# Kernel tuning notes

Hardware: AMD Instinct MI355X
Metric: run time of the kernel (lower is better)

Reference implementation:

```python
import jax, jax.numpy as jnp
import numpy as np

B, N1, N2 = 4, 2048, 8192
F_IN, F_OUT = 256, 256
K = 3          # PyG knn_interpolate default
BN_EPS = 1e-5


def linear_bn(x, W, b, gamma, beta):
    # Linear + BatchNorm1d (training mode: batch stats over B*N per feature)
    h = jnp.einsum('bni,io->bno', x, W) + b
    mean = h.mean(axis=(0, 1))
    var = h.var(axis=(0, 1))
    xhat = (h - mean) * jax.lax.rsqrt(var + BN_EPS)
    return gamma * xhat + beta


def knn_interpolate(f1, p1, p2):
    # f1: [N1,F], p1: [N1,3], p2: [N2,3] -> [N2,F]
    d2 = jnp.sum((p2[:, None, :] - p1[None, :, :]) ** 2, axis=-1)  # [N2,N1]
    neg_d2, idx = jax.lax.top_k(-d2, K)                            # k smallest
    w = 1.0 / jnp.maximum(-neg_d2, 1e-16)                          # [N2,K]
    fk = f1[idx]                                                   # [N2,K,F]
    return jnp.sum(w[..., None] * fk, axis=1) / jnp.sum(w, axis=1, keepdims=True)


def setup_inputs() -> dict:
    key = jax.random.key(0)
    ks = jax.random.split(key, 10)
    return {
        'features_1': jax.random.normal(ks[0], (B, N1, F_IN), jnp.float32),
        'positions_1': jax.random.uniform(ks[1], (B, N1, 3), jnp.float32),
        'batch_1': jnp.repeat(jnp.arange(B, dtype=jnp.int64), N1),
        'features_2': jax.random.normal(ks[2], (B, N2, F_IN), jnp.float32),
        'positions_2': jax.random.uniform(ks[3], (B, N2, 3), jnp.float32),
        'batch_2': jnp.repeat(jnp.arange(B, dtype=jnp.int64), N2),
        'W1': jax.random.normal(ks[4], (F_IN, F_OUT), jnp.float32) * (1.0 / np.sqrt(F_IN)),
        'b1': jax.random.normal(ks[5], (F_OUT,), jnp.float32) * 0.02,
        'gamma1': jnp.ones((F_OUT,), jnp.float32),
        'beta1': jnp.zeros((F_OUT,), jnp.float32),
        'W2': jax.random.normal(ks[6], (F_IN, F_OUT), jnp.float32) * (1.0 / np.sqrt(F_IN)),
        'b2': jax.random.normal(ks[7], (F_OUT,), jnp.float32) * 0.02,
        'gamma2': jnp.ones((F_OUT,), jnp.float32),
        'beta2': jnp.zeros((F_OUT,), jnp.float32),
    }


def reference(features_1, positions_1, batch_1, features_2, positions_2, batch_2,
              W1, b1, gamma1, beta1, W2, b2, gamma2, beta2):
    f1 = linear_bn(features_1, W1, b1, gamma1, beta1)          # [B,N1,F_OUT]
    f2 = linear_bn(features_2, W2, b2, gamma2, beta2)          # [B,N2,F_OUT]
    # batch structure is regular [B,N]: knn restricted within batch == vmap over B
    interp = jax.vmap(knn_interpolate)(f1, positions_1, positions_2)  # [B,N2,F_OUT]
    return (interp + f2, positions_2, batch_2)
```

## Files before the change

kernel.cpp:

```cpp
#include <hip/hip_runtime.h>
#include <math.h>

#define BATCH   4
#define N1      2048
#define N2      8192
#define F       256
#define NTOT1   (BATCH * N1)
#define NTOT2   (BATCH * N2)
#define BN_EPS  1e-5f

typedef __attribute__((ext_vector_type(8))) short bf16x8;
typedef __attribute__((ext_vector_type(4))) float f32x4;

__device__ __forceinline__ unsigned short f2bf(float f) {
    unsigned u = __float_as_uint(f);
    unsigned r = (u + 0x7fffu + ((u >> 16) & 1u)) >> 16;
    return (unsigned short)r;
}
__device__ __forceinline__ float bflo(unsigned u) {
    return __uint_as_float(u << 16);
}
__device__ __forceinline__ float bfhi(unsigned u) {
    return __uint_as_float(u & 0xffff0000u);
}
__device__ __forceinline__ void async16(const void* g, void* l) {
    __builtin_amdgcn_global_load_lds(
        (const __attribute__((address_space(1))) unsigned int*)g,
        (__attribute__((address_space(3))) unsigned int*)l, 16, 0, 0);
}

__device__ __forceinline__ void ins3m(float d, int j,
                                      float& d0, float& d1, float& d2,
                                      int& j0, int& j1, int& j2) {
    const bool c0 = d < d0;
    const bool c1 = d < d1;
    const bool c2 = d < d2;
    const float nd1 = __builtin_amdgcn_fmed3f(d, d0, d1);
    const float nd2 = __builtin_amdgcn_fmed3f(d, d1, d2);
    d0 = fminf(d, d0);
    d1 = nd1;
    d2 = nd2;
    j2 = c1 ? j1 : (c2 ? j : j2);
    j1 = c0 ? j0 : (c1 ? j : j1);
    j0 = c0 ? j  : j0;
}

__global__ __launch_bounds__(256) void prep_kernel(const float4* __restrict__ f1,
                                                   const float4* __restrict__ f2,
                                                   const float* __restrict__ W1,
                                                   const float* __restrict__ W2,
                                                   ushort4* __restrict__ Xb1,
                                                   ushort4* __restrict__ Xb2,
                                                   unsigned short* __restrict__ Wt1,
                                                   unsigned short* __restrict__ Wt2,
                                                   float* __restrict__ sums) {
    const int bx = blockIdx.x;
    const int t  = threadIdx.x;

    if (bx < 8192) {
        const int i = bx * 256 + t;
        const float4 v = f2[i];
        ushort4 o;
        o.x = f2bf(v.x); o.y = f2bf(v.y); o.z = f2bf(v.z); o.w = f2bf(v.w);
        Xb2[i] = o;
    } else if (bx < 10240) {
        const int i = (bx - 8192) * 256 + t;
        const float4 v = f1[i];
        ushort4 o;
        o.x = f2bf(v.x); o.y = f2bf(v.y); o.z = f2bf(v.z); o.w = f2bf(v.w);
        Xb1[i] = o;
    } else if (bx < 10272) {
        __shared__ float tile[64][65];
        const int bb = bx - 10240;
        const bool second = bb >= 16;
        const int bl = second ? bb - 16 : bb;
        const float* W = second ? W2 : W1;
        unsigned short* Wt = second ? Wt2 : Wt1;
        const int gx0 = (bl & 3) * 64;
        const int gy0 = (bl >> 2) * 64;
        const int tx = t & 63;
        const int ty = t >> 6;
        #pragma unroll
        for (int j = 0; j < 16; ++j) {
            const int row = ty * 16 + j;
            tile[row][tx] = W[(size_t)(gy0 + row) * 256 + gx0 + tx];
        }
        __syncthreads();
        #pragma unroll
        for (int j = 0; j < 16; ++j) {
            const int row = ty * 16 + j;
            Wt[(size_t)(gx0 + row) * 256 + gy0 + tx] = f2bf(tile[tx][row]);
        }
    } else {
        #pragma unroll
        for (int i = 0; i < 4; ++i) sums[t + 256 * i] = 0.0f;
    }
}

__global__ __launch_bounds__(256) void gemm_mfma_kernel(const unsigned short* __restrict__ Xb1,
                                                        const unsigned short* __restrict__ Xb2,
                                                        const unsigned short* __restrict__ Wt1,
                                                        const unsigned short* __restrict__ Wt2,
                                                        const float* __restrict__ b1,
                                                        const float* __restrict__ b2,
                                                        unsigned short* __restrict__ h1b,
                                                        unsigned short* __restrict__ h2b,
                                                        float* __restrict__ sums) {
    __shared__ unsigned short As[128 * 32];
    __shared__ unsigned short Bs[128 * 32];

    const int bx   = blockIdx.x;
    const bool g2  = bx >= 64;
    const unsigned short* Xb = g2 ? Xb2 : Xb1;
    const unsigned short* Wt = g2 ? Wt2 : Wt1;
    const float* bias        = g2 ? b2 : b1;
    unsigned short* Hb       = g2 ? h2b : h1b;
    float* sum               = sums + (g2 ? 512 : 0);
    float* sumsq             = sum + 256;
    const int row0 = (g2 ? bx - 64 : bx) * 128;
    const int n0   = blockIdx.y * 128;

    const int t    = threadIdx.x;
    const int wave = t >> 6;
    const int lane = t & 63;
    const int wm   = (wave & 1) * 64;
    const int wn   = (wave >> 1) * 64;
    const int ml   = lane & 15;
    const int q    = lane >> 4;

    f32x4 acc[4][4] = {};

    for (int kt = 0; kt < 256; kt += 32) {
        #pragma unroll
        for (int r = 0; r < 2; ++r) {
            const int e   = r * 2048 + t * 8;
            const int row = e >> 5;
            const int kk  = e & 31;
            async16(Xb + (size_t)(row0 + row) * 256 + kt + kk, (unsigned short*)As + e);
            async16(Wt + (size_t)(n0 + row) * 256 + kt + kk, (unsigned short*)Bs + e);
        }
        __syncthreads();

        bf16x8 af[4], bfr[4];
        #pragma unroll
        for (int mt = 0; mt < 4; ++mt)
            af[mt] = *(const bf16x8*)&As[(wm + mt * 16 + ml) * 32 + q * 8];
        #pragma unroll
        for (int nt = 0; nt < 4; ++nt)
            bfr[nt] = *(const bf16x8*)&Bs[(wn + nt * 16 + ml) * 32 + q * 8];
        #pragma unroll
        for (int mt = 0; mt < 4; ++mt)
            #pragma unroll
            for (int nt = 0; nt < 4; ++nt)
                acc[mt][nt] = __builtin_amdgcn_mfma_f32_16x16x32_bf16(af[mt], bfr[nt],
                                                                      acc[mt][nt], 0, 0, 0);
        __syncthreads();
    }

    float bv[4], psum[4], psq[4];
    #pragma unroll
    for (int nt = 0; nt < 4; ++nt) {
        bv[nt] = bias[n0 + wn + nt * 16 + ml];
        psum[nt] = 0.0f; psq[nt] = 0.0f;
    }
    #pragma unroll
    for (int mt = 0; mt < 4; ++mt)
        #pragma unroll
        for (int nt = 0; nt < 4; ++nt)
            #pragma unroll
            for (int r = 0; r < 4; ++r) {
                const float v = acc[mt][nt][r] + bv[nt];
                const int grow = row0 + wm + mt * 16 + q * 4 + r;
                Hb[(size_t)grow * 256 + n0 + wn + nt * 16 + ml] = f2bf(v);
                psum[nt] += v;
                psq[nt]  = fmaf(v, v, psq[nt]);
            }
    #pragma unroll
    for (int nt = 0; nt < 4; ++nt) {
        psum[nt] += __shfl_xor(psum[nt], 16, 64);
        psum[nt] += __shfl_xor(psum[nt], 32, 64);
        psq[nt]  += __shfl_xor(psq[nt], 16, 64);
        psq[nt]  += __shfl_xor(psq[nt], 32, 64);
    }
    if (q == 0) {
        #pragma unroll
        for (int nt = 0; nt < 4; ++nt) {
            const int col = n0 + wn + nt * 16 + ml;
            atomicAdd(&sum[col],   psum[nt]);
            atomicAdd(&sumsq[col], psq[nt]);
        }
    }
}

__global__ __launch_bounds__(512) void fused_kernel(const float* __restrict__ p1,
                                                    const float* __restrict__ p2,
                                                    const unsigned short* __restrict__ h1b,
                                                    const unsigned short* __restrict__ h2b,
                                                    const float* __restrict__ sums,
                                                    const float* __restrict__ g1,
                                                    const float* __restrict__ be1,
                                                    const float* __restrict__ g2,
                                                    const float* __restrict__ be2,
                                                    float* __restrict__ out) {
    __shared__ float px[N1], py[N1], pz[N1];
    __shared__ float pdl[8][64][3];
    __shared__ int   pil[8][64][3];
    __shared__ float wql[64][3];
    __shared__ int   jql[64][3];
    __shared__ float ssl[4][256];

    const int t     = threadIdx.x;
    const int bx    = blockIdx.x;
    const int qbase = bx * 64;
    const int b     = bx >> 7;
    const int wave  = t >> 6;
    const int lane  = t & 63;

    #pragma unroll
    for (int r = 0; r < 4; ++r) {
        const int j = r * 512 + t;
        const size_t base = (size_t)(b * N1 + j) * 3;
        px[j] = p1[base + 0];
        py[j] = p1[base + 1];
        pz[j] = p1[base + 2];
    }
    if (t < 256) {
        const float m1 = sums[t] * (1.0f / (float)NTOT1);
        const float v1 = sums[256 + t] * (1.0f / (float)NTOT1) - m1 * m1;
        const float s1 = g1[t] * rsqrtf(v1 + BN_EPS);
        ssl[0][t] = s1;
        ssl[1][t] = be1[t] - m1 * s1;
        const float m2 = sums[512 + t] * (1.0f / (float)NTOT2);
        const float v2 = sums[768 + t] * (1.0f / (float)NTOT2) - m2 * m2;
        const float s2 = g2[t] * rsqrtf(v2 + BN_EPS);
        ssl[2][t] = s2;
        ssl[3][t] = be2[t] - m2 * s2;
    }
    __syncthreads();

    {
        const int iq = qbase + lane;
        const float qx = p2[(size_t)iq * 3 + 0];
        const float qy = p2[(size_t)iq * 3 + 1];
        const float qz = p2[(size_t)iq * 3 + 2];

        float d0 = 1e30f, d1 = 1e30f, d2 = 1e30f;
        int   i0 = 0,     i1 = 0,     i2 = 0;

        const int jb = wave * 256;
        #pragma unroll 2
        for (int jj = 0; jj < 256; jj += 4) {
            const float4 x4 = *(const float4*)&px[jb + jj];
            const float4 y4 = *(const float4*)&py[jb + jj];
            const float4 z4 = *(const float4*)&pz[jb + jj];
            {
                const float dx = x4.x - qx, dy = y4.x - qy, dz = z4.x - qz;
                float d = dx * dx; d = fmaf(dy, dy, d); d = fmaf(dz, dz, d);
                ins3m(d, jj + 0, d0, d1, d2, i0, i1, i2);
            }
            {
                const float dx = x4.y - qx, dy = y4.y - qy, dz = z4.y - qz;
                float d = dx * dx; d = fmaf(dy, dy, d); d = fmaf(dz, dz, d);
                ins3m(d, jj + 1, d0, d1, d2, i0, i1, i2);
            }
            {
                const float dx = x4.z - qx, dy = y4.z - qy, dz = z4.z - qz;
                float d = dx * dx; d = fmaf(dy, dy, d); d = fmaf(dz, dz, d);
                ins3m(d, jj + 2, d0, d1, d2, i0, i1, i2);
            }
            {
                const float dx = x4.w - qx, dy = y4.w - qy, dz = z4.w - qz;
                float d = dx * dx; d = fmaf(dy, dy, d); d = fmaf(dz, dz, d);
                ins3m(d, jj + 3, d0, d1, d2, i0, i1, i2);
            }
        }
        pdl[wave][lane][0] = d0; pdl[wave][lane][1] = d1; pdl[wave][lane][2] = d2;
        pil[wave][lane][0] = jb + i0; pil[wave][lane][1] = jb + i1; pil[wave][lane][2] = jb + i2;
    }
    __syncthreads();

    if (t < 64) {
        float d0 = 1e30f, d1 = 1e30f, d2 = 1e30f;
        int   j0 = 0,     j1 = 0,     j2 = 0;
        #pragma unroll
        for (int s = 0; s < 8; ++s)
            #pragma unroll
            for (int k = 0; k < 3; ++k)
                ins3m(pdl[s][t][k], pil[s][t][k], d0, d1, d2, j0, j1, j2);

        const float w0 = 1.0f / fmaxf(d0, 1e-16f);
        const float w1 = 1.0f / fmaxf(d1, 1e-16f);
        const float w2 = 1.0f / fmaxf(d2, 1e-16f);
        const float inv = 1.0f / (w0 + w1 + w2);
        wql[t][0] = w0 * inv; wql[t][1] = w1 * inv; wql[t][2] = w2 * inv;
        jql[t][0] = b * N1 + j0; jql[t][1] = b * N1 + j1; jql[t][2] = b * N1 + j2;
    }
    __syncthreads();

    {
        const int fp = t & 127;
        const int f0 = fp * 2;
        const int qg = t >> 7;
        const float s1a = ssl[0][f0], t1a = ssl[1][f0];
        const float s2a = ssl[2][f0], t2a = ssl[3][f0];
        const float s1b = ssl[0][f0 + 1], t1b = ssl[1][f0 + 1];
        const float s2b = ssl[2][f0 + 1], t2b = ssl[3][f0 + 1];

        for (int qq = 0; qq < 16; ++qq) {
            const int v = qg * 16 + qq;
            const int i = qbase + v;
            const int   j0 = jql[v][0], j1 = jql[v][1], j2 = jql[v][2];
            const float w0 = wql[v][0], w1 = wql[v][1], w2 = wql[v][2];

            const unsigned u0 = *(const unsigned*)(h1b + (size_t)j0 * F + f0);
            const unsigned u1 = *(const unsigned*)(h1b + (size_t)j1 * F + f0);
            const unsigned u2 = *(const unsigned*)(h1b + (size_t)j2 * F + f0);
            const unsigned uh = *(const unsigned*)(h2b + (size_t)i * F + f0);

            float alo = w0 * bflo(u0);
            alo = fmaf(w1, bflo(u1), alo);
            alo = fmaf(w2, bflo(u2), alo);
            float ahi = w0 * bfhi(u0);
            ahi = fmaf(w1, bfhi(u1), ahi);
            ahi = fmaf(w2, bfhi(u2), ahi);

            float2 o;
            o.x = fmaf(alo, s1a, t1a) + fmaf(bflo(uh), s2a, t2a);
            o.y = fmaf(ahi, s1b, t1b) + fmaf(bfhi(uh), s2b, t2b);
            *(float2*)(out + (size_t)i * F + f0) = o;
        }
    }

    if (t < 256) {
        const int tid = bx * 256 + t;
        if (tid < NTOT2 * 3) {
            out[(size_t)NTOT2 * F + tid] = p2[tid];
        } else {
            const int e = tid - NTOT2 * 3;
            out[(size_t)NTOT2 * F + NTOT2 * 3 + e] = (float)(e >> 13);
        }
    }
}

extern "C" void kernel_launch(void* const* d_in, const int* in_sizes, int n_in,
                              void* d_out, int out_size, void* d_ws, size_t ws_size,
                              hipStream_t stream) {
    const float* f1  = (const float*)d_in[0];
    const float* p1  = (const float*)d_in[1];
    const float* f2  = (const float*)d_in[3];
    const float* p2  = (const float*)d_in[4];
    const float* W1  = (const float*)d_in[6];
    const float* b1  = (const float*)d_in[7];
    const float* g1  = (const float*)d_in[8];
    const float* be1 = (const float*)d_in[9];
    const float* W2  = (const float*)d_in[10];
    const float* b2  = (const float*)d_in[11];
    const float* g2  = (const float*)d_in[12];
    const float* be2 = (const float*)d_in[13];

    char* ws = (char*)d_ws;
    unsigned short* Xb1  = (unsigned short*)(ws);
    unsigned short* Xb2  = (unsigned short*)(ws + 4194304);
    unsigned short* Wt1  = (unsigned short*)(ws + 20971520);
    unsigned short* Wt2  = (unsigned short*)(ws + 21102592);
    unsigned short* h1b  = (unsigned short*)(ws + 21233664);
    unsigned short* h2b  = (unsigned short*)(ws + 25427968);
    float*          sums = (float*)(ws + 42205184);
    float*          out  = (float*)d_out;

    prep_kernel<<<10273, 256, 0, stream>>>((const float4*)f1, (const float4*)f2,
                                           W1, W2, (ushort4*)Xb1, (ushort4*)Xb2,
                                           Wt1, Wt2, sums);

    dim3 gg(320, 2);
    gemm_mfma_kernel<<<gg, 256, 0, stream>>>(Xb1, Xb2, Wt1, Wt2, b1, b2,
                                             h1b, h2b, sums);

    fused_kernel<<<512, 512, 0, stream>>>(p1, p2, h1b, h2b, sums,
                                          g1, be1, g2, be2, out);
}
```

Measured before the change: 182.7 us.

## Replace brute-force kNN with uniform 6x6x6 grid search and expanding shells

Builds a per-batch uniform spatial grid for source points and buckets query points by cell inside the prep kernel. The fused kernel then assigns one block per (batch, cell), scans neighbouring cells in growing shells, and stops once the third-nearest distance is within the distance to the box boundary. This replaces the O(N1) brute-force distance scan per query with a local search. In exchange it adds counting-sort passes, uneven per-block work and extra synchronisation, and the grid bounds assume positions lie in [0,1].

```diff
diff --git a/kernel.cpp b/kernel.cpp
--- a/kernel.cpp
+++ b/kernel.cpp
@@ -8,6 +8,11 @@
 #define NTOT1   (BATCH * N1)
 #define NTOT2   (BATCH * N2)
 #define BN_EPS  1e-5f
+
+#define GR      6
+#define NC      216
+#define NCP     (NC + 1)
+#define GH      (1.0f / 6.0f)
 
 typedef __attribute__((ext_vector_type(8))) short bf16x8;
 typedef __attribute__((ext_vector_type(4))) float f32x4;
@@ -45,15 +50,29 @@
     j0 = c0 ? j  : j0;
 }
 
+__device__ __forceinline__ int clamp6(int c) { return c < 0 ? 0 : (c > 5 ? 5 : c); }
+__device__ __forceinline__ int cell_of(float x, float y, float z) {
+    const int cx = clamp6((int)(x * 6.0f));
+    const int cy = clamp6((int)(y * 6.0f));
+    const int cz = clamp6((int)(z * 6.0f));
+    return (cz * 6 + cy) * 6 + cx;
+}
+
 __global__ __launch_bounds__(256) void prep_kernel(const float4* __restrict__ f1,
                                                    const float4* __restrict__ f2,
                                                    const float* __restrict__ W1,
                                                    const float* __restrict__ W2,
+                                                   const float* __restrict__ p1,
+                                                   const float* __restrict__ p2,
                                                    ushort4* __restrict__ Xb1,
                                                    ushort4* __restrict__ Xb2,
                                                    unsigned short* __restrict__ Wt1,
                                                    unsigned short* __restrict__ Wt2,
-                                                   float* __restrict__ sums) {
+                                                   float* __restrict__ sums,
+                                                   float4* __restrict__ gridPts,
+                                                   int* __restrict__ cellStart,
+                                                   int* __restrict__ qSorted,
+                                                   int* __restrict__ qCellStart) {
     const int bx = blockIdx.x;
     const int t  = threadIdx.x;
 
@@ -91,9 +110,79 @@
             const int row = ty * 16 + j;
             Wt[(size_t)(gx0 + row) * 256 + gy0 + tx] = f2bf(tile[tx][row]);
         }
+    } else if (bx == 10272) {
+        #pragma unroll
+        for (int i = 0; i < 4; ++i) sums[t + 256 * i] = 0.0f;
+    } else if (bx < 10277) {
+        __shared__ int cnt[NC];
+        __shared__ int ofs[NCP];
+        const int b = bx - 10273;
+        if (t < NC) cnt[t] = 0;
+        __syncthreads();
+        int   myc[8];
+        float mx[8], my[8], mz[8];
+        #pragma unroll
+        for (int r = 0; r < 8; ++r) {
+            const int i = r * 256 + t;
+            const size_t base = (size_t)(b * N1 + i) * 3;
+            mx[r] = p1[base]; my[r] = p1[base + 1]; mz[r] = p1[base + 2];
+            myc[r] = cell_of(mx[r], my[r], mz[r]);
+            atomicAdd(&cnt[myc[r]], 1);
+        }
+        __syncthreads();
+        if (t <= NC) ofs[t] = (t == 0) ? 0 : cnt[t - 1];
+        __syncthreads();
+        for (int dd = 1; dd < NCP; dd <<= 1) {
+            int v = 0;
+            if (t <= NC && t >= dd) v = ofs[t - dd];
+            __syncthreads();
+            if (t <= NC && t >= dd) ofs[t] += v;
+            __syncthreads();
+        }
+        if (t < NC) cnt[t] = ofs[t];
+        __syncthreads();
+        #pragma unroll
+        for (int r = 0; r < 8; ++r) {
+            const int i = r * 256 + t;
+            const int pos = atomicAdd(&cnt[myc[r]], 1);
+            float4 rec;
+            rec.x = mx[r]; rec.y = my[r]; rec.z = mz[r];
+            rec.w = __int_as_float(i);
+            gridPts[(size_t)b * N1 + pos] = rec;
+        }
+        if (t <= NC) cellStart[b * NCP + t] = ofs[t];
     } else {
-        #pragma unroll
-        for (int i = 0; i < 4; ++i) sums[t + 256 * i] = 0.0f;
+        __shared__ int cnt[NC];
+        __shared__ int ofs[NCP];
+        const int b = bx - 10277;
+        if (t < NC) cnt[t] = 0;
+        __syncthreads();
+        for (int r = 0; r < 32; ++r) {
+            const int i = r * 256 + t;
+            const size_t base = (size_t)(b * N2 + i) * 3;
+            const int c = cell_of(p2[base], p2[base + 1], p2[base + 2]);
+            atomicAdd(&cnt[c], 1);
+        }
+        __syncthreads();
+        if (t <= NC) ofs[t] = (t == 0) ? 0 : cnt[t - 1];
+        __syncthreads();
+        for (int dd = 1; dd < NCP; dd <<= 1) {
+            int v = 0;
+            if (t <= NC && t >= dd) v = ofs[t - dd];
+            __syncthreads();
+            if (t <= NC && t >= dd) ofs[t] += v;
+            __syncthreads();
+        }
+        if (t < NC) cnt[t] = ofs[t];
+        __syncthreads();
+        for (int r = 0; r < 32; ++r) {
+            const int i = r * 256 + t;
+            const size_t base = (size_t)(b * N2 + i) * 3;
+            const int c = cell_of(p2[base], p2[base + 1], p2[base + 2]);
+            const int pos = atomicAdd(&cnt[c], 1);
+            qSorted[(size_t)b * N2 + pos] = b * N2 + i;
+        }
+        if (t <= NC) qCellStart[b * NCP + t] = ofs[t];
     }
 }
 
@@ -192,8 +281,7 @@
     }
 }
 
-__global__ __launch_bounds__(512) void fused_kernel(const float* __restrict__ p1,
-                                                    const float* __restrict__ p2,
+__global__ __launch_bounds__(512) void fused_kernel(const float* __restrict__ p2,
                                                     const unsigned short* __restrict__ h1b,
                                                     const unsigned short* __restrict__ h2b,
                                                     const float* __restrict__ sums,
@@ -201,29 +289,32 @@
                                                     const float* __restrict__ be1,
                                                     const float* __restrict__ g2,
                                                     const float* __restrict__ be2,
+                                                    const float4* __restrict__ gridPts,
+                                                    const int* __restrict__ cellStart,
+                                                    const int* __restrict__ qSorted,
+                                                    const int* __restrict__ qCellStart,
                                                     float* __restrict__ out) {
-    __shared__ float px[N1], py[N1], pz[N1];
+    __shared__ float ssl[4][256];
+    __shared__ int   cst[NCP];
     __shared__ float pdl[8][64][3];
     __shared__ int   pil[8][64][3];
+    __shared__ float qdl[64][3];
+    __shared__ int   qjl[64][3];
     __shared__ float wql[64][3];
     __shared__ int   jql[64][3];
-    __shared__ float ssl[4][256];
-
-    const int t     = threadIdx.x;
-    const int bx    = blockIdx.x;
-    const int qbase = bx * 64;
-    const int b     = bx >> 7;
-    const int wave  = t >> 6;
-    const int lane  = t & 63;
-
-    #pragma unroll
-    for (int r = 0; r < 4; ++r) {
-        const int j = r * 512 + t;
-        const size_t base = (size_t)(b * N1 + j) * 3;
-        px[j] = p1[base + 0];
-        py[j] = p1[base + 1];
-        pz[j] = p1[base + 2];
-    }
+    __shared__ int   qidl[64];
+    __shared__ float qpx[64], qpy[64], qpz[64];
+
+    const int t    = threadIdx.x;
+    const int bx   = blockIdx.x;
+    const int b    = bx / NC;
+    const int cid  = bx - b * NC;
+    const int ccx  = cid % 6;
+    const int ccy  = (cid / 6) % 6;
+    const int ccz  = cid / 36;
+    const int wave = t >> 6;
+    const int lane = t & 63;
+
     if (t < 256) {
         const float m1 = sums[t] * (1.0f / (float)NTOT1);
         const float v1 = sums[256 + t] * (1.0f / (float)NTOT1) - m1 * m1;
@@ -236,106 +327,178 @@
         ssl[2][t] = s2;
         ssl[3][t] = be2[t] - m2 * s2;
     }
-    __syncthreads();
-
-    {
-        const int iq = qbase + lane;
-        const float qx = p2[(size_t)iq * 3 + 0];
-        const float qy = p2[(size_t)iq * 3 + 1];
-        const float qz = p2[(size_t)iq * 3 + 2];
-
-        float d0 = 1e30f, d1 = 1e30f, d2 = 1e30f;
-        int   i0 = 0,     i1 = 0,     i2 = 0;
-
-        const int jb = wave * 256;
-        #pragma unroll 2
-        for (int jj = 0; jj < 256; jj += 4) {
-            const float4 x4 = *(const float4*)&px[jb + jj];
-            const float4 y4 = *(const float4*)&py[jb + jj];
-            const float4 z4 = *(const float4*)&pz[jb + jj];
-            {
-                const float dx = x4.x - qx, dy = y4.x - qy, dz = z4.x - qz;
-                float d = dx * dx; d = fmaf(dy, dy, d); d = fmaf(dz, dz, d);
-                ins3m(d, jj + 0, d0, d1, d2, i0, i1, i2);
+    if (t < NCP) cst[t] = cellStart[b * NCP + t];
+
+    const int qs = qCellStart[b * NCP + cid];
+    const int qe = qCellStart[b * NCP + cid + 1];
+    const float4* __restrict__ gp = gridPts + (size_t)b * N1;
+
+    for (int q0 = qs; q0 < qe; q0 += 64) {
+        const int nqc = min(64, qe - q0);
+        __syncthreads();
+        if (t < 64) {
+            int qid = 0;
+            float x = 1e30f, y = 1e30f, z = 1e30f;
+            if (t < nqc) {
+                qid = qSorted[(size_t)b * N2 + q0 + t];
+                const size_t pb = (size_t)qid * 3;
+                x = p2[pb]; y = p2[pb + 1]; z = p2[pb + 2];
             }
-            {
-                const float dx = x4.y - qx, dy = y4.y - qy, dz = z4.y - qz;
-                float d = dx * dx; d = fmaf(dy, dy, d); d = fmaf(dz, dz, d);
-                ins3m(d, jj + 1, d0, d1, d2, i0, i1, i2);
+            qidl[t] = qid;
+            qpx[t] = x; qpy[t] = y; qpz[t] = z;
+        }
+        __syncthreads();
+
+        const float qx = qpx[lane], qy = qpy[lane], qz = qpz[lane];
+
+        auto scan_box = [&](int R, float& d0, float& d1, float& d2,
+                            int& i0, int& i1, int& i2) {
+            const int dim  = 2 * R + 1;
+            const int dim2 = dim * dim;
+            const int nsl  = dim2 * dim;
+            for (int sl = wave; sl < nsl; sl += 8) {
+                int lz = sl / dim2;
+                const int rem = sl - lz * dim2;
+                int ly = rem / dim;
+                int lx = rem - ly * dim;
+                lx -= R; ly -= R; lz -= R;
+                if (R > 1) {
+                    const int ax = lx < 0 ? -lx : lx;
+                    const int ay = ly < 0 ? -ly : ly;
+                    const int az = lz < 0 ? -lz : lz;
+                    int ch = ax > ay ? ax : ay;
+                    ch = ch > az ? ch : az;
+                    if (ch < R) continue;
+                }
+                const int gx = ccx + lx;
+                const int gy = ccy + ly;
+                const int gz = ccz + lz;
+                if ((unsigned)gx >= 6u || (unsigned)gy >= 6u || (unsigned)gz >= 6u)
+                    continue;
+                const int cc = (gz * 6 + gy) * 6 + gx;
+                const int s = __builtin_amdgcn_readfirstlane(cst[cc]);
+                const int e = __builtin_amdgcn_readfirstlane(cst[cc + 1]);
+                for (int j = s; j < e; ++j) {
+                    const float4 p = gp[j];
+                    const float dx = p.x - qx;
+                    const float dy = p.y - qy;
+                    const float dz = p.z - qz;
+                    float d = dx * dx;
+                    d = fmaf(dy, dy, d);
+                    d = fmaf(dz, dz, d);
+                    ins3m(d, __float_as_int(p.w), d0, d1, d2, i0, i1, i2);
+                }
             }
-            {
-                const float dx = x4.z - qx, dy = y4.z - qy, dz = z4.z - qz;
-                float d = dx * dx; d = fmaf(dy, dy, d); d = fmaf(dz, dz, d);
-                ins3m(d, jj + 2, d0, d1, d2, i0, i1, i2);
+        };
+
+        auto merge_check = [&](int R) -> int {
+            int notdone = 0;
+            if (t < 64) {
+                float m0, m1, m2;
+                int a0, a1, a2;
+                if (R == 1) { m0 = m1 = m2 = 1e30f; a0 = a1 = a2 = 0; }
+                else {
+                    m0 = qdl[t][0]; m1 = qdl[t][1]; m2 = qdl[t][2];
+                    a0 = qjl[t][0]; a1 = qjl[t][1]; a2 = qjl[t][2];
+                }
+                #pragma unroll
+                for (int s = 0; s < 8; ++s)
+                    #pragma unroll
+                    for (int k = 0; k < 3; ++k)
+                        ins3m(pdl[s][t][k], pil[s][t][k], m0, m1, m2, a0, a1, a2);
+                qdl[t][0] = m0; qdl[t][1] = m1; qdl[t][2] = m2;
+                qjl[t][0] = a0; qjl[t][1] = a1; qjl[t][2] = a2;
+                if (t < nqc) {
+                    float dmin = 1e30f;
+                    {
+                        const int lo = ccx - R, hi = ccx + R;
+                        if (lo > 0) dmin = fminf(dmin, qpx[t] - (float)lo * GH);
+                        if (hi < 5) dmin = fminf(dmin, (float)(hi + 1) * GH - qpx[t]);
+                    }
+                    {
+                        const int lo = ccy - R, hi = ccy + R;
+                        if (lo > 0) dmin = fminf(dmin, qpy[t] - (float)lo * GH);
+                        if (hi < 5) dmin = fminf(dmin, (float)(hi + 1) * GH - qpy[t]);
+                    }
+                    {
+                        const int lo = ccz - R, hi = ccz + R;
+                        if (lo > 0) dmin = fminf(dmin, qpz[t] - (float)lo * GH);
+                        if (hi < 5) dmin = fminf(dmin, (float)(hi + 1) * GH - qpz[t]);
+                    }
+                    if (m2 > dmin * dmin * 0.9999f) notdone = 1;
+                }
             }
-            {
-                const float dx = x4.w - qx, dy = y4.w - qy, dz = z4.w - qz;
-                float d = dx * dx; d = fmaf(dy, dy, d); d = fmaf(dz, dz, d);
-                ins3m(d, jj + 3, d0, d1, d2, i0, i1, i2);
+            return __syncthreads_count(notdone);
+        };
+
+        {
+            float d0 = 1e30f, d1 = 1e30f, d2 = 1e30f;
+            int i0 = 0, i1 = 0, i2 = 0;
+            scan_box(1, d0, d1, d2, i0, i1, i2);
+            pdl[wave][lane][0] = d0; pdl[wave][lane][1] = d1; pdl[wave][lane][2] = d2;
+            pil[wave][lane][0] = i0; pil[wave][lane][1] = i1; pil[wave][lane][2] = i2;
+        }
+        __syncthreads();
+        int need = merge_check(1);
+        for (int R = 2; need != 0 && R <= 6; ++R) {
+            float d0 = 1e30f, d1 = 1e30f, d2 = 1e30f;
+            int i0 = 0, i1 = 0, i2 = 0;
+            scan_box(R, d0, d1, d2, i0, i1, i2);
+            pdl[wave][lane][0] = d0; pdl[wave][lane][1] = d1; pdl[wave][lane][2] = d2;
+            pil[wave][lane][0] = i0; pil[wave][lane][1] = i1; pil[wave][lane][2] = i2;
+            __syncthreads();
+            need = merge_check(R);
+        }
+
+        if (t < nqc) {
+            const float w0 = 1.0f / fmaxf(qdl[t][0], 1e-16f);
+            const float w1 = 1.0f / fmaxf(qdl[t][1], 1e-16f);
+            const float w2 = 1.0f / fmaxf(qdl[t][2], 1e-16f);
+            const float inv = 1.0f / (w0 + w1 + w2);
+            wql[t][0] = w0 * inv; wql[t][1] = w1 * inv; wql[t][2] = w2 * inv;
+            jql[t][0] = b * N1 + qjl[t][0];
+            jql[t][1] = b * N1 + qjl[t][1];
+            jql[t][2] = b * N1 + qjl[t][2];
+        }
+        __syncthreads();
+
+        {
+            const int fp = t & 127;
+            const int f0 = fp * 2;
+            const float s1a = ssl[0][f0],     t1a = ssl[1][f0];
+            const float s2a = ssl[2][f0],     t2a = ssl[3][f0];
+            const float s1b = ssl[0][f0 + 1], t1b = ssl[1][f0 + 1];
+            const float s2b = ssl[2][f0 + 1], t2b = ssl[3][f0 + 1];
+            for (int v = t >> 7; v < nqc; v += 4) {
+                const int qid = qidl[v];
+                const int   j0 = jql[v][0], j1 = jql[v][1], j2 = jql[v][2];
+                const float w0 = wql[v][0], w1 = wql[v][1], w2 = wql[v][2];
+
+                const unsigned u0 = *(const unsigned*)(h1b + (size_t)j0 * F + f0);
+                const unsigned u1 = *(const unsigned*)(h1b + (size_t)j1 * F + f0);
+                const unsigned u2 = *(const unsigned*)(h1b + (size_t)j2 * F + f0);
+                const unsigned uh = *(const unsigned*)(h2b + (size_t)qid * F + f0);
+
+                float alo = w0 * bflo(u0);
+                alo = fmaf(w1, bflo(u1), alo);
+                alo = fmaf(w2, bflo(u2), alo);
+                float ahi = w0 * bfhi(u0);
+                ahi = fmaf(w1, bfhi(u1), ahi);
+                ahi = fmaf(w2, bfhi(u2), ahi);
+
+                float2 o;
+                o.x = fmaf(alo, s1a, t1a) + fmaf(bflo(uh), s2a, t2a);
+                o.y = fmaf(ahi, s1b, t1b) + fmaf(bfhi(uh), s2b, t2b);
+                *(float2*)(out + (size_t)qid * F + f0) = o;
             }
         }
-        pdl[wave][lane][0] = d0; pdl[wave][lane][1] = d1; pdl[wave][lane][2] = d2;
-        pil[wave][lane][0] = jb + i0; pil[wave][lane][1] = jb + i1; pil[wave][lane][2] = jb + i2;
-    }
-    __syncthreads();
-
-    if (t < 64) {
-        float d0 = 1e30f, d1 = 1e30f, d2 = 1e30f;
-        int   j0 = 0,     j1 = 0,     j2 = 0;
-        #pragma unroll
-        for (int s = 0; s < 8; ++s)
-            #pragma unroll
-            for (int k = 0; k < 3; ++k)
-                ins3m(pdl[s][t][k], pil[s][t][k], d0, d1, d2, j0, j1, j2);
-
-        const float w0 = 1.0f / fmaxf(d0, 1e-16f);
-        const float w1 = 1.0f / fmaxf(d1, 1e-16f);
-        const float w2 = 1.0f / fmaxf(d2, 1e-16f);
-        const float inv = 1.0f / (w0 + w1 + w2);
-        wql[t][0] = w0 * inv; wql[t][1] = w1 * inv; wql[t][2] = w2 * inv;
-        jql[t][0] = b * N1 + j0; jql[t][1] = b * N1 + j1; jql[t][2] = b * N1 + j2;
-    }
-    __syncthreads();
-
-    {
-        const int fp = t & 127;
-        const int f0 = fp * 2;
-        const int qg = t >> 7;
-        const float s1a = ssl[0][f0], t1a = ssl[1][f0];
-        const float s2a = ssl[2][f0], t2a = ssl[3][f0];
-        const float s1b = ssl[0][f0 + 1], t1b = ssl[1][f0 + 1];
-        const float s2b = ssl[2][f0 + 1], t2b = ssl[3][f0 + 1];
-
-        for (int qq = 0; qq < 16; ++qq) {
-            const int v = qg * 16 + qq;
-            const int i = qbase + v;
-            const int   j0 = jql[v][0], j1 = jql[v][1], j2 = jql[v][2];
-            const float w0 = wql[v][0], w1 = wql[v][1], w2 = wql[v][2];
-
-            const unsigned u0 = *(const unsigned*)(h1b + (size_t)j0 * F + f0);
-            const unsigned u1 = *(const unsigned*)(h1b + (size_t)j1 * F + f0);
-            const unsigned u2 = *(const unsigned*)(h1b + (size_t)j2 * F + f0);
-            const unsigned uh = *(const unsigned*)(h2b + (size_t)i * F + f0);
-
-            float alo = w0 * bflo(u0);
-            alo = fmaf(w1, bflo(u1), alo);
-            alo = fmaf(w2, bflo(u2), alo);
-            float ahi = w0 * bfhi(u0);
-            ahi = fmaf(w1, bfhi(u1), ahi);
-            ahi = fmaf(w2, bfhi(u2), ahi);
-
-            float2 o;
-            o.x = fmaf(alo, s1a, t1a) + fmaf(bflo(uh), s2a, t2a);
-            o.y = fmaf(ahi, s1b, t1b) + fmaf(bfhi(uh), s2b, t2b);
-            *(float2*)(out + (size_t)i * F + f0) = o;
-        }
-    }
-
-    if (t < 256) {
-        const int tid = bx * 256 + t;
+    }
+
+    if (t < 152) {
+        const int tid = bx * 152 + t;
         if (tid < NTOT2 * 3) {
             out[(size_t)NTOT2 * F + tid] = p2[tid];
-        } else {
+        } else if (tid < NTOT2 * 3 + NTOT2) {
             const int e = tid - NTOT2 * 3;
             out[(size_t)NTOT2 * F + NTOT2 * 3 + e] = (float)(e >> 13);
         }
@@ -359,23 +522,31 @@
     const float* be2 = (const float*)d_in[13];
 
     char* ws = (char*)d_ws;
-    unsigned short* Xb1  = (unsigned short*)(ws);
-    unsigned short* Xb2  = (unsigned short*)(ws + 4194304);
-    unsigned short* Wt1  = (unsigned short*)(ws + 20971520);
-    unsigned short* Wt2  = (unsigned short*)(ws + 21102592);
-    unsigned short* h1b  = (unsigned short*)(ws + 21233664);
-    unsigned short* h2b  = (unsigned short*)(ws + 25427968);
-    float*          sums = (float*)(ws + 42205184);
-    float*          out  = (float*)d_out;
-
-    prep_kernel<<<10273, 256, 0, stream>>>((const float4*)f1, (const float4*)f2,
-                                           W1, W2, (ushort4*)Xb1, (ushort4*)Xb2,
-                                           Wt1, Wt2, sums);
+    unsigned short* Xb1   = (unsigned short*)(ws);
+    unsigned short* Xb2   = (unsigned short*)(ws + 4194304);
+    unsigned short* Wt1   = (unsigned short*)(ws + 20971520);
+    unsigned short* Wt2   = (unsigned short*)(ws + 21102592);
+    unsigned short* h1b   = (unsigned short*)(ws + 21233664);
+    unsigned short* h2b   = (unsigned short*)(ws + 25427968);
+    float*          sums  = (float*)(ws + 42205184);
+    float4*         gridPts    = (float4*)(ws + 42209280);
+    int*            cellStart  = (int*)(ws + 42340352);
+    int*            qSorted    = (int*)(ws + 42343936);
+    int*            qCellStart = (int*)(ws + 42475008);
+    float*          out   = (float*)d_out;
+
+    prep_kernel<<<10281, 256, 0, stream>>>((const float4*)f1, (const float4*)f2,
+                                           W1, W2, p1, p2,
+                                           (ushort4*)Xb1, (ushort4*)Xb2,
+                                           Wt1, Wt2, sums,
+                                           gridPts, cellStart, qSorted, qCellStart);
 
     dim3 gg(320, 2);
     gemm_mfma_kernel<<<gg, 256, 0, stream>>>(Xb1, Xb2, Wt1, Wt2, b1, b2,
                                              h1b, h2b, sums);
 
-    fused_kernel<<<512, 512, 0, stream>>>(p1, p2, h1b, h2b, sums,
-                                          g1, be1, g2, be2, out);
-}
+    fused_kernel<<<864, 512, 0, stream>>>(p2, h1b, h2b, sums,
+                                          g1, be1, g2, be2,
+                                          gridPts, cellStart, qSorted, qCellStart,
+                                          out);
+}
```

Result: slower. 188.7 us (+3.3%).
